# Performance work log

Hardware: AMD Instinct MI355X
Metric: run time of the kernel (lower is better)

## Reference

```python
import jax, jax.numpy as jnp
import numpy as np


def hardsigmoid(x):
    # relu6(x + 3) / 6
    return jnp.clip(x + 3.0, 0.0, 6.0) / 6.0


def setup_inputs() -> dict:
    key = jax.random.key(0)
    k1, k2 = jax.random.split(key)
    x = jax.random.normal(k1, (16, 256, 128, 128), dtype=jnp.float32)
    # Conv2d(2, 1, kernel_size=3, bias=False): weight [out=1, in=2, 3, 3]
    fan_in = 2 * 3 * 3
    bound = 1.0 / np.sqrt(fan_in)
    conv_w = jax.random.uniform(k2, (1, 2, 3, 3), minval=-bound, maxval=bound, dtype=jnp.float32)
    return {"x": x, "conv_w": conv_w}


def reference(x, conv_w):
    # x: [B, C, H, W]
    avg_out = jnp.mean(x, axis=1, keepdims=True)   # [B,1,H,W]
    max_out = jnp.max(x, axis=1, keepdims=True)    # [B,1,H,W]
    y = jnp.concatenate([avg_out, max_out], axis=1)  # [B,2,H,W]
    y = jax.lax.conv_general_dilated(
        y, conv_w,
        window_strides=(1, 1),
        padding=((1, 1), (1, 1)),
        dimension_numbers=("NCHW", "OIHW", "NCHW"),
    )  # [B,1,H,W]
    y = hardsigmoid(y)
    return x * y
```

## Files before the change

### kernel.cpp

```cpp
#include <hip/hip_runtime.h>
#include <math.h>

#define BB 16
#define CC 256
#define HH 128
#define WW 128
#define HWP (HH * WW)
#define PLANE ((size_t)CC * HWP)

__global__ __launch_bounds__(256) void reduce_kernel(
    const float* __restrict__ x,
    float* __restrict__ avg_map,
    float* __restrict__ max_map)
{
    int t  = blockIdx.x * blockDim.x + threadIdx.x;
    int b  = t / (HWP / 2);
    int p2 = t % (HWP / 2);

    const float2* xp = (const float2*)(x + (size_t)b * PLANE) + p2;

    float2 s = make_float2(0.f, 0.f);
    float2 m = make_float2(-INFINITY, -INFINITY);
    #pragma unroll 8
    for (int c = 0; c < CC; ++c) {
        float2 v = xp[c * (HWP / 2)];
        s.x += v.x;               s.y += v.y;
        m.x = fmaxf(m.x, v.x);    m.y = fmaxf(m.y, v.y);
    }

    float2* ap = (float2*)(avg_map + (size_t)b * HWP) + p2;
    float2* mp = (float2*)(max_map + (size_t)b * HWP) + p2;
    *ap = make_float2(s.x * (1.f / 256.f), s.y * (1.f / 256.f));
    *mp = m;
}

__global__ __launch_bounds__(256) void apply_kernel(
    const float* __restrict__ x,
    const float* __restrict__ cw,
    const float* __restrict__ avg_map,
    const float* __restrict__ max_map,
    float* __restrict__ out)
{
    int t  = blockIdx.x * blockDim.x + threadIdx.x;
    int b  = t / (HWP / 2);
    int p2 = t % (HWP / 2);
    int h  = p2 / (WW / 2);
    int w0 = (p2 % (WW / 2)) * 2;

    float wa[9], wm[9];
    #pragma unroll
    for (int i = 0; i < 9; ++i) { wa[i] = cw[i]; wm[i] = cw[9 + i]; }

    const float* am = avg_map + (size_t)b * HWP;
    const float* mm = max_map + (size_t)b * HWP;

    float acc0 = 0.f, acc1 = 0.f;
    #pragma unroll
    for (int ki = 0; ki < 3; ++ki) {
        int hh = h + ki - 1;
        if (hh < 0 || hh >= HH) continue;
        #pragma unroll
        for (int kj = 0; kj < 3; ++kj) {
            float fa = wa[ki * 3 + kj];
            float fm = wm[ki * 3 + kj];
            int wwa = w0 + kj - 1;
            int wwb = w0 + 1 + kj - 1;
            if (wwa >= 0 && wwa < WW)
                acc0 += fa * am[hh * WW + wwa] + fm * mm[hh * WW + wwa];
            if (wwb >= 0 && wwb < WW)
                acc1 += fa * am[hh * WW + wwb] + fm * mm[hh * WW + wwb];
        }
    }

    float a0 = fminf(fmaxf(acc0 + 3.f, 0.f), 6.f) * (1.f / 6.f);
    float a1 = fminf(fmaxf(acc1 + 3.f, 0.f), 6.f) * (1.f / 6.f);

    const float2* xp = (const float2*)(x + (size_t)b * PLANE) + p2;
    float2*       op = (float2*)(out + (size_t)b * PLANE) + p2;
    #pragma unroll 8
    for (int c = 0; c < CC; ++c) {
        float2 v = xp[c * (HWP / 2)];
        op[c * (HWP / 2)] = make_float2(v.x * a0, v.y * a1);
    }
}

extern "C" void kernel_launch(void* const* d_in, const int* in_sizes, int n_in,
                              void* d_out, int out_size, void* d_ws, size_t ws_size,
                              hipStream_t stream)
{
    const float* x  = (const float*)d_in[0];
    const float* cw = (const float*)d_in[1];
    float* out      = (float*)d_out;

    float* avg_map = (float*)d_ws;
    float* max_map = avg_map + (size_t)BB * HWP;

    const int total_f2 = BB * HWP / 2;
    const int block    = 256;
    const int grid     = total_f2 / block;

    reduce_kernel<<<grid, block, 0, stream>>>(x, avg_map, max_map);
    apply_kernel <<<grid, block, 0, stream>>>(x, cw, avg_map, max_map, out);
}
```

Baseline: 512.9 us.

## Split channel reduction, separate conv kernel, vectorize apply with nontemporal float4

```diff
diff --git a/kernel.cpp b/kernel.cpp
--- a/kernel.cpp
+++ b/kernel.cpp
@@ -6,81 +6,99 @@
 #define HH 128
 #define WW 128
 #define HWP (HH * WW)
+#define P4  (HWP / 4)
 #define PLANE ((size_t)CC * HWP)
+
+typedef float f4 __attribute__((ext_vector_type(4)));
 
 __global__ __launch_bounds__(256) void reduce_kernel(
     const float* __restrict__ x,
-    float* __restrict__ avg_map,
-    float* __restrict__ max_map)
+    float* __restrict__ psum,
+    float* __restrict__ pmax)
 {
-    int t  = blockIdx.x * blockDim.x + threadIdx.x;
-    int b  = t / (HWP / 2);
-    int p2 = t % (HWP / 2);
+    int t    = blockIdx.x * 256 + threadIdx.x;
+    int p4   = t & (P4 - 1);
+    int half = (t >> 12) & 1;
+    int b    = t >> 13;
 
-    const float2* xp = (const float2*)(x + (size_t)b * PLANE) + p2;
+    const f4* xp = (const f4*)(x + (size_t)b * PLANE + (size_t)half * 128 * HWP) + p4;
 
-    float2 s = make_float2(0.f, 0.f);
-    float2 m = make_float2(-INFINITY, -INFINITY);
+    f4 s = {0.f, 0.f, 0.f, 0.f};
+    f4 m = {-INFINITY, -INFINITY, -INFINITY, -INFINITY};
     #pragma unroll 8
-    for (int c = 0; c < CC; ++c) {
-        float2 v = xp[c * (HWP / 2)];
-        s.x += v.x;               s.y += v.y;
-        m.x = fmaxf(m.x, v.x);    m.y = fmaxf(m.y, v.y);
+    for (int c = 0; c < 128; ++c) {
+        f4 v = xp[c * P4];
+        s.x += v.x; s.y += v.y; s.z += v.z; s.w += v.w;
+        m.x = fmaxf(m.x, v.x); m.y = fmaxf(m.y, v.y);
+        m.z = fmaxf(m.z, v.z); m.w = fmaxf(m.w, v.w);
     }
 
-    float2* ap = (float2*)(avg_map + (size_t)b * HWP) + p2;
-    float2* mp = (float2*)(max_map + (size_t)b * HWP) + p2;
-    *ap = make_float2(s.x * (1.f / 256.f), s.y * (1.f / 256.f));
+    f4* sp = (f4*)(psum + ((size_t)half * BB + b) * HWP) + p4;
+    f4* mp = (f4*)(pmax + ((size_t)half * BB + b) * HWP) + p4;
+    *sp = s;
     *mp = m;
 }
 
-__global__ __launch_bounds__(256) void apply_kernel(
-    const float* __restrict__ x,
+__global__ __launch_bounds__(256) void conv_kernel(
     const float* __restrict__ cw,
-    const float* __restrict__ avg_map,
-    const float* __restrict__ max_map,
-    float* __restrict__ out)
+    const float* __restrict__ psum,
+    const float* __restrict__ pmax,
+    float* __restrict__ amap)
 {
-    int t  = blockIdx.x * blockDim.x + threadIdx.x;
-    int b  = t / (HWP / 2);
-    int p2 = t % (HWP / 2);
-    int h  = p2 / (WW / 2);
-    int w0 = (p2 % (WW / 2)) * 2;
+    int t  = blockIdx.x * 256 + threadIdx.x;
+    int hw = t & (HWP - 1);
+    int b  = t >> 14;
+    int h  = hw >> 7;
+    int w  = hw & (WW - 1);
 
     float wa[9], wm[9];
     #pragma unroll
     for (int i = 0; i < 9; ++i) { wa[i] = cw[i]; wm[i] = cw[9 + i]; }
 
-    const float* am = avg_map + (size_t)b * HWP;
-    const float* mm = max_map + (size_t)b * HWP;
+    const float* s0 = psum + (size_t)b * HWP;
+    const float* s1 = psum + ((size_t)BB + b) * HWP;
+    const float* m0 = pmax + (size_t)b * HWP;
+    const float* m1 = pmax + ((size_t)BB + b) * HWP;
 
-    float acc0 = 0.f, acc1 = 0.f;
+    float acc = 0.f;
     #pragma unroll
     for (int ki = 0; ki < 3; ++ki) {
         int hh = h + ki - 1;
         if (hh < 0 || hh >= HH) continue;
         #pragma unroll
         for (int kj = 0; kj < 3; ++kj) {
-            float fa = wa[ki * 3 + kj];
-            float fm = wm[ki * 3 + kj];
-            int wwa = w0 + kj - 1;
-            int wwb = w0 + 1 + kj - 1;
-            if (wwa >= 0 && wwa < WW)
-                acc0 += fa * am[hh * WW + wwa] + fm * mm[hh * WW + wwa];
-            if (wwb >= 0 && wwb < WW)
-                acc1 += fa * am[hh * WW + wwb] + fm * mm[hh * WW + wwb];
+            int ww = w + kj - 1;
+            if (ww < 0 || ww >= WW) continue;
+            int n = hh * WW + ww;
+            float avg = (s0[n] + s1[n]) * (1.f / 256.f);
+            float mx  = fmaxf(m0[n], m1[n]);
+            acc += wa[ki * 3 + kj] * avg + wm[ki * 3 + kj] * mx;
         }
     }
+    amap[t] = fminf(fmaxf(acc + 3.f, 0.f), 6.f) * (1.f / 6.f);
+}
 
-    float a0 = fminf(fmaxf(acc0 + 3.f, 0.f), 6.f) * (1.f / 6.f);
-    float a1 = fminf(fmaxf(acc1 + 3.f, 0.f), 6.f) * (1.f / 6.f);
+__global__ __launch_bounds__(256) void apply_kernel(
+    const float* __restrict__ x,
+    const float* __restrict__ amap,
+    float* __restrict__ out)
+{
+    int t  = blockIdx.x * 256 + threadIdx.x;
+    int p4 = t & (P4 - 1);
+    int g  = (t >> 12) & 3;
+    int b  = t >> 14;
 
-    const float2* xp = (const float2*)(x + (size_t)b * PLANE) + p2;
-    float2*       op = (float2*)(out + (size_t)b * PLANE) + p2;
+    f4 a = *((const f4*)(amap + (size_t)b * HWP) + p4);
+
+    const f4* xp = (const f4*)(x   + (size_t)b * PLANE + (size_t)g * 64 * HWP) + p4;
+    f4*       op = (f4*)      (out + (size_t)b * PLANE + (size_t)g * 64 * HWP) + p4;
+
     #pragma unroll 8
-    for (int c = 0; c < CC; ++c) {
-        float2 v = xp[c * (HWP / 2)];
-        op[c * (HWP / 2)] = make_float2(v.x * a0, v.y * a1);
+    for (int ci = 63; ci >= 0; --ci) {
+        f4 v = __builtin_nontemporal_load(xp + ci * P4);
+        f4 r;
+        r.x = v.x * a.x; r.y = v.y * a.y; r.z = v.z * a.z; r.w = v.w * a.w;
+        __builtin_nontemporal_store(r, op + ci * P4);
     }
 }
 
@@ -92,13 +110,11 @@
     const float* cw = (const float*)d_in[1];
     float* out      = (float*)d_out;
 
-    float* avg_map = (float*)d_ws;
-    float* max_map = avg_map + (size_t)BB * HWP;
+    float* psum = (float*)d_ws;
+    float* pmax = psum + (size_t)2 * BB * HWP;
+    float* amap = pmax + (size_t)2 * BB * HWP;
 
-    const int total_f2 = BB * HWP / 2;
-    const int block    = 256;
-    const int grid     = total_f2 / block;
-
-    reduce_kernel<<<grid, block, 0, stream>>>(x, avg_map, max_map);
-    apply_kernel <<<grid, block, 0, stream>>>(x, cw, avg_map, max_map, out);
+    reduce_kernel<<<512,  256, 0, stream>>>(x, psum, pmax);
+    conv_kernel  <<<1024, 256, 0, stream>>>(cw, psum, pmax, amap);
+    apply_kernel <<<1024, 256, 0, stream>>>(x, amap, out);
 }
```

Result: faster. 497.4 us (-3.0%).
